# Optimization experiments

Hardware: AMD Instinct MI355X
Metric: run time of the kernel (lower is better)

## Reference

```python
import jax, jax.numpy as jnp
import numpy as np

N_NODES = 100000
EMBED_DIM = 256


def _sage_conv(x, src, dst, W_l, b_l, W_r, num_nodes):
    # PyG SAGEConv (mean aggr): out = lin_l(mean_{j in N(i)} x_j) + lin_r(x_i)
    msg = x[src]                                              # [E, D] gather
    agg = jax.ops.segment_sum(msg, dst, num_segments=num_nodes)   # [N, D]
    cnt = jax.ops.segment_sum(jnp.ones((src.shape[0], 1), x.dtype), dst,
                              num_segments=num_nodes)         # [N, 1]
    mean = agg / jnp.maximum(cnt, 1.0)
    return mean @ W_l + b_l + x @ W_r


def setup_inputs() -> dict:
    key = jax.random.key(0)
    ks = jax.random.split(key, 12)
    D = EMBED_DIM
    glorot = 1.0 / np.sqrt(D)
    inp = {
        "emb": jax.random.uniform(ks[0], (N_NODES + 1, D), jnp.float32, 0.001, 0.3),
        "W1l": jax.random.uniform(ks[1], (D, D), jnp.float32, -glorot, glorot),
        "b1l": jnp.zeros((D,), jnp.float32),
        "W1r": jax.random.uniform(ks[2], (D, D), jnp.float32, -glorot, glorot),
        "W2l": jax.random.uniform(ks[3], (D, D), jnp.float32, -glorot, glorot),
        "b2l": jnp.zeros((D,), jnp.float32),
        "W2r": jax.random.uniform(ks[4], (D, D), jnp.float32, -glorot, glorot),
        "x_idx": jax.random.randint(ks[5], (N_NODES,), 0, N_NODES + 1, jnp.int64 if jax.config.read('jax_enable_x64') else jnp.int32),
        "edge_index": jax.random.randint(ks[6], (2, 1600000), 0, N_NODES, jnp.int32),
        "drugNodes": jax.random.randint(ks[7], (1024,), 0, N_NODES, jnp.int32),
        "seNodes": jax.random.randint(ks[8], (1024,), 0, N_NODES, jnp.int32),
    }
    return inp


def reference(emb, W1l, b1l, W1r, W2l, b2l, W2r, x_idx, edge_index, drugNodes, seNodes):
    src, dst = edge_index[0], edge_index[1]
    x = emb[x_idx]                                            # embedding lookup [N, D]
    x = _sage_conv(x, src, dst, W1l, b1l, W1r, x.shape[0])
    x = _sage_conv(x, src, dst, W2l, b2l, W2r, x.shape[0])
    drugEmbedding = x[drugNodes]
    seEmbedding = x[seNodes]
    return (drugEmbedding, seEmbedding, x)
```

## Files before the change

kernel.cpp:

```cpp
#include <hip/hip_runtime.h>
#include <hip/hip_bf16.h>


typedef __bf16 bf16x8 __attribute__((ext_vector_type(8)));
typedef __bf16 bf16x4 __attribute__((ext_vector_type(4)));
typedef float  f32x4  __attribute__((ext_vector_type(4)));
typedef float  f32x8  __attribute__((ext_vector_type(8)));

#define ROWB 1024
#define NPART 256
#define MAXBUK 2048

__device__ __forceinline__ void async_copy16(void* lds_dst, const void* g_src) {
  __builtin_amdgcn_global_load_lds(
      (const __attribute__((address_space(1))) void*)g_src,
      (__attribute__((address_space(3))) void*)lds_dst, 16, 0, 0);
}


__global__ void bin_count(const int* __restrict__ dst, int* __restrict__ hmat,
                          int E, int chunk, int nbuk) {
  __shared__ int lh[MAXBUK];
  int p = blockIdx.x, tid = threadIdx.x;
  for (int i = tid; i < nbuk; i += 256) lh[i] = 0;
  __syncthreads();
  int base = p * chunk, end = min(base + chunk, E);
  for (int e = base + tid; e < end; e += 256) atomicAdd(&lh[dst[e] >> 6], 1);
  __syncthreads();
  for (int i = tid; i < nbuk; i += 256) hmat[p * nbuk + i] = lh[i];
}

__global__ void col_scan(int* __restrict__ hmat, int* __restrict__ btot, int nbuk) {
  __shared__ int s[NPART];
  int b = blockIdx.x, t = threadIdx.x;
  int v = hmat[t * nbuk + b];
  s[t] = v; __syncthreads();
  for (int d = 1; d < NPART; d <<= 1) {
    int add = (t >= d) ? s[t - d] : 0;
    __syncthreads();
    s[t] += add;
    __syncthreads();
  }
  hmat[t * nbuk + b] = s[t] - v;
  if (t == NPART - 1) btot[b] = s[t];
}

__global__ void bucket_scan(const int* __restrict__ btot, int* __restrict__ boff, int nb) {
  __shared__ int s[2048];
  int t = threadIdx.x;
  for (int i = t; i < 2048; i += 1024) s[i] = (i < nb) ? btot[i] : 0;
  __syncthreads();
  for (int d = 1; d < 2048; d <<= 1) {
    int v0 = (t >= d) ? s[t - d] : 0;
    int v1 = (t + 1024 >= d) ? s[t + 1024 - d] : 0;
    __syncthreads();
    s[t] += v0; s[t + 1024] += v1;
    __syncthreads();
  }
  for (int i = t; i < nb; i += 1024) boff[i] = s[i] - btot[i];
}

__global__ void part_write(const int* __restrict__ src, const int* __restrict__ dst,
                           const int* __restrict__ hmat, const int* __restrict__ boff,
                           int* __restrict__ ebuf, int E, int chunk, int nbuk) {
  __shared__ int cur[MAXBUK];
  int p = blockIdx.x, tid = threadIdx.x;
  for (int i = tid; i < nbuk; i += 256) cur[i] = hmat[p * nbuk + i] + boff[i];
  __syncthreads();
  int base = p * chunk, end = min(base + chunk, E);
  for (int e = base + tid; e < end; e += 256) {
    int d = dst[e];
    int pos = atomicAdd(&cur[d >> 6], 1);
    ebuf[pos] = src[e] | ((d & 63) << 18);
  }
}

__global__ void node_hist_scan(const int* __restrict__ ebuf, const int* __restrict__ boff,
                               const int* __restrict__ btot, int* __restrict__ cnt,
                               int* __restrict__ offs, int N) {
  __shared__ int lh[64];
  int b = blockIdx.x, tid = threadIdx.x;
  if (tid < 64) lh[tid] = 0;
  __syncthreads();
  int s0 = boff[b], s1 = s0 + btot[b];
  for (int i = s0 + tid; i < s1; i += 256) atomicAdd(&lh[ebuf[i] >> 18], 1);
  __syncthreads();
  if (tid < 64) {
    int v = lh[tid];
    int x = v;
#pragma unroll
    for (int d = 1; d < 64; d <<= 1) {
      int y = __shfl_up(x, d);
      if (tid >= d) x += y;
    }
    int node = b * 64 + tid;
    if (node < N) { cnt[node] = v; offs[node] = s0 + x - v; }
  }
}

__global__ void csr_write(const int* __restrict__ ebuf, const int* __restrict__ boff,
                          const int* __restrict__ btot, const int* __restrict__ offs,
                          int* __restrict__ csr, int N) {
  __shared__ int cur[64];
  int b = blockIdx.x, tid = threadIdx.x;
  int node = b * 64 + tid;
  if (tid < 64) cur[tid] = (node < N) ? offs[node] : 0;
  __syncthreads();
  int s0 = boff[b], s1 = s0 + btot[b];
  for (int i = s0 + tid; i < s1; i += 256) {
    int e = ebuf[i];
    int p = atomicAdd(&cur[e >> 18], 1);
    csr[p] = e & 0x3FFFF;
  }
}


__global__ void prep_w_kernel(const float* __restrict__ W1l, const float* __restrict__ W1r,
                              const float* __restrict__ W2l, const float* __restrict__ W2r,
                              __bf16* __restrict__ Wt1, __bf16* __restrict__ Wt2) {
  int idx = blockIdx.x * 256 + threadIdx.x;
  int which = idx >> 17;
  int j = idx & 131071;
  int n = j >> 9, k = j & 511;
  const float* Wl = which ? W2l : W1l;
  const float* Wr = which ? W2r : W1r;
  float v = (k < 256) ? Wl[k * 256 + n] : Wr[(k - 256) * 256 + n];
  (which ? Wt2 : Wt1)[j] = (__bf16)v;
}

__global__ void gather_x_kernel(const float* __restrict__ emb, const int* __restrict__ x_idx,
                                char* __restrict__ xbase, int N) {
  int wave = threadIdx.x >> 6, lane = threadIdx.x & 63;
  int i = blockIdx.x * 4 + wave;
  if (i >= N) return;
  int s = x_idx[i];
  float4 v = *(const float4*)(emb + (size_t)s * 256 + lane * 4);
  bf16x4 o = { (__bf16)v.x, (__bf16)v.y, (__bf16)v.z, (__bf16)v.w };
  *(bf16x4*)(xbase + (size_t)i * ROWB + lane * 8) = o;
}


__global__ void sage_agg(const char* __restrict__ srcbase,
                         char* __restrict__ dstbase,
                         const int* __restrict__ csr, const int* __restrict__ cnt,
                         const int* __restrict__ offs, int N) {
  int wave = threadIdx.x >> 6, lane = threadIdx.x & 63;
  int i = blockIdx.x * 4 + wave;
  if (i >= N) return;
  int deg = cnt[i];
  const int* lp = csr + offs[i];
  int half = lane >> 5, l5 = lane & 31;
  const char* sb = srcbase + l5 * 16;

  f32x8 acc = (f32x8)0.f;
  int g8 = deg >> 3;
  for (int t = 0; t < g8; ++t) {
    const int* p = lp + t * 8 + half;
    int s0 = p[0], s1 = p[2], s2 = p[4], s3 = p[6];
    bf16x8 v0 = *(const bf16x8*)(sb + (size_t)s0 * ROWB);
    bf16x8 v1 = *(const bf16x8*)(sb + (size_t)s1 * ROWB);
    bf16x8 v2 = *(const bf16x8*)(sb + (size_t)s2 * ROWB);
    bf16x8 v3 = *(const bf16x8*)(sb + (size_t)s3 * ROWB);
#pragma unroll
    for (int k = 0; k < 8; ++k)
      acc[k] += ((float)v0[k] + (float)v1[k]) + ((float)v2[k] + (float)v3[k]);
  }
  int base = g8 * 8;
  int rem = deg & 7;
  int rp = rem >> 1;
  for (int u = 0; u < rp; ++u) {
    int r0 = lp[base + 2 * u + half];
    bf16x8 v0 = *(const bf16x8*)(sb + (size_t)r0 * ROWB);
#pragma unroll
    for (int k = 0; k < 8; ++k) acc[k] += (float)v0[k];
  }
  if ((rem & 1) && half == 0) {
    int r0 = lp[deg - 1];
    bf16x8 v0 = *(const bf16x8*)(sb + (size_t)r0 * ROWB);
#pragma unroll
    for (int k = 0; k < 8; ++k) acc[k] += (float)v0[k];
  }

  float inv = 1.0f / (float)(deg > 0 ? deg : 1);
  bf16x8 o;
#pragma unroll
  for (int k = 0; k < 8; ++k) {
    float s = acc[k] + __shfl_down(acc[k], 32);
    o[k] = (__bf16)(s * inv);
  }
  if (half == 0)
    *(bf16x8*)(dstbase + (size_t)i * ROWB + l5 * 16) = o;
}


template <int OUT_F32>
__global__ __launch_bounds__(256) void gemm_sage(const char* __restrict__ Abase,
                                                 const __bf16* __restrict__ Wt,
                                                 const float* __restrict__ bias,
                                                 char* __restrict__ outbase, int M) {
  __shared__ __align__(16) char lds[49152];
  const int tid = threadIdx.x;
  const int wave = tid >> 6, lane = tid & 63;
  const int r = lane & 15, q = lane >> 4;
  const int wm = wave >> 1, wn = wave & 1;
  const int row0 = blockIdx.x * 128;

  f32x4 acc[4][8];
#pragma unroll
  for (int t = 0; t < 4; ++t)
#pragma unroll
    for (int u = 0; u < 8; ++u) acc[t][u] = (f32x4)0.f;

  auto stage = [&](int kk, int buf) {
    char* lbase = lds + buf * 24576;
#pragma unroll
    for (int i = 0; i < 2; ++i) {
      int h = wave * 2 + i;
      int rowA = row0 + h * 16 + r;
      rowA = rowA < M ? rowA : M - 1;
      async_copy16(lbase + h * 1024 + lane * 16,
                   Abase + (size_t)rowA * ROWB + (size_t)(kk * 32 + q * 8) * 2);
    }
#pragma unroll
    for (int i = 0; i < 4; ++i) {
      int h = wave * 4 + i;
      async_copy16(lbase + 8192 + h * 1024 + lane * 16,
                   (const char*)Wt + ((size_t)(h * 16 + r) * 512 + kk * 32 + q * 8) * 2);
    }
  };

  stage(0, 0);
  for (int kk = 0; kk < 16; ++kk) {
    __syncthreads();
    if (kk < 15) stage(kk + 1, (kk + 1) & 1);
    const char* lbase = lds + (kk & 1) * 24576;
    bf16x8 a[4];
#pragma unroll
    for (int t = 0; t < 4; ++t)
      a[t] = *(const bf16x8*)(lbase + (wm * 4 + t) * 1024 + lane * 16);
#pragma unroll
    for (int u = 0; u < 8; ++u) {
      bf16x8 b = *(const bf16x8*)(lbase + 8192 + (wn * 8 + u) * 1024 + lane * 16);
#pragma unroll
      for (int t = 0; t < 4; ++t)
        acc[t][u] = __builtin_amdgcn_mfma_f32_16x16x32_bf16(a[t], b, acc[t][u], 0, 0, 0);
    }
  }

#pragma unroll
  for (int t = 0; t < 4; ++t) {
    int rbase = row0 + wm * 64 + t * 16 + q * 4;
#pragma unroll
    for (int u = 0; u < 8; ++u) {
      int col = wn * 128 + u * 16 + r;
      float bv = bias[col];
#pragma unroll
      for (int j = 0; j < 4; ++j) {
        int row = rbase + j;
        if (row < M) {
          float v = acc[t][u][j] + bv;
          if (OUT_F32)
            *(float*)(outbase + (size_t)row * ROWB + col * 4) = v;
          else
            *(__bf16*)(outbase + (size_t)row * ROWB + 512 + col * 2) = (__bf16)v;
        }
      }
    }
  }
}


__global__ void gather_out_kernel(const float* __restrict__ x2, const int* __restrict__ drug,
                                  const int* __restrict__ se, float* __restrict__ out,
                                  int nd, int ns) {
  int wave = threadIdx.x >> 6, lane = threadIdx.x & 63;
  int ro = blockIdx.x * 4 + wave;
  if (ro >= nd + ns) return;
  int node = (ro < nd) ? drug[ro] : se[ro - nd];
  float4 v = *(const float4*)(x2 + (size_t)node * 256 + lane * 4);
  *(float4*)(out + (size_t)ro * 256 + lane * 4) = v;
}


extern "C" void kernel_launch(void* const* d_in, const int* in_sizes, int n_in,
                              void* d_out, int out_size, void* d_ws, size_t ws_size,
                              hipStream_t stream) {
  const float* emb  = (const float*)d_in[0];
  const float* W1l  = (const float*)d_in[1];
  const float* b1l  = (const float*)d_in[2];
  const float* W1r  = (const float*)d_in[3];
  const float* W2l  = (const float*)d_in[4];
  const float* b2l  = (const float*)d_in[5];
  const float* W2r  = (const float*)d_in[6];
  const int* x_idx  = (const int*)d_in[7];
  const int* edge   = (const int*)d_in[8];
  const int* drug   = (const int*)d_in[9];
  const int* se     = (const int*)d_in[10];

  const int N = in_sizes[7];
  const int E = in_sizes[8] / 2;
  const int nd = in_sizes[9], ns = in_sizes[10];
  const int* esrc = edge;
  const int* edst = edge + E;
  const int NBUK = (N + 63) >> 6;
  const int chunk = (E + NPART - 1) / NPART;

  char* ws = (char*)d_ws;
  size_t off = 0;
  char* xA1 = ws;                       off += (size_t)((N + 127) & ~127) * ROWB;
  __bf16* Wt1 = (__bf16*)(ws + off);    off += 512 * 256 * 2;
  __bf16* Wt2 = (__bf16*)(ws + off);    off += 512 * 256 * 2;
  int* cnt  = (int*)(ws + off);         off += ((size_t)N * 4 + 255) & ~(size_t)255;
  int* offs = (int*)(ws + off);         off += ((size_t)N * 4 + 255) & ~(size_t)255;
  int* csr  = (int*)(ws + off);         off += ((size_t)E * 4 + 255) & ~(size_t)255;
  int* ebuf = (int*)xA1;
  int* hmat = (int*)(xA1 + (8u << 20));
  int* btot = (int*)(xA1 + (16u << 20));
  int* boff = (int*)(xA1 + (16u << 20) + 16384);

  float* outp = (float*)d_out;
  float* x2 = outp + (size_t)(nd + ns) * 256;
  char* scratch2 = (char*)x2;

  const int QB = (N + 3) / 4;
  const int GB = (N + 127) / 128;

  prep_w_kernel<<<(2 * 131072) / 256, 256, 0, stream>>>(W1l, W1r, W2l, W2r, Wt1, Wt2);

  bin_count<<<NPART, 256, 0, stream>>>(edst, hmat, E, chunk, NBUK);
  col_scan<<<NBUK, NPART, 0, stream>>>(hmat, btot, NBUK);
  bucket_scan<<<1, 1024, 0, stream>>>(btot, boff, NBUK);
  part_write<<<NPART, 256, 0, stream>>>(esrc, edst, hmat, boff, ebuf, E, chunk, NBUK);
  node_hist_scan<<<NBUK, 256, 0, stream>>>(ebuf, boff, btot, cnt, offs, N);
  csr_write<<<NBUK, 256, 0, stream>>>(ebuf, boff, btot, offs, csr, N);

  gather_x_kernel<<<QB, 256, 0, stream>>>(emb, x_idx, xA1 + 512, N);
  sage_agg<<<QB, 256, 0, stream>>>(xA1 + 512, xA1, csr, cnt, offs, N);
  gemm_sage<0><<<GB, 256, 0, stream>>>(xA1, Wt1, b1l, scratch2, N);
  sage_agg<<<QB, 256, 0, stream>>>(scratch2 + 512, scratch2, csr, cnt, offs, N);
  gemm_sage<1><<<GB, 256, 0, stream>>>(scratch2, Wt2, b2l, scratch2, N);

  gather_out_kernel<<<(nd + ns + 3) / 4, 256, 0, stream>>>(x2, drug, se, outp, nd, ns);
}
```

Baseline: 639.0 us.

## Load GEMM operands directly into registers and fuse node histogram with CSR write

```diff
diff --git a/kernel.cpp b/kernel.cpp
--- a/kernel.cpp
+++ b/kernel.cpp
@@ -10,12 +10,6 @@
 #define ROWB 1024
 #define NPART 256
 #define MAXBUK 2048
-
-__device__ __forceinline__ void async_copy16(void* lds_dst, const void* g_src) {
-  __builtin_amdgcn_global_load_lds(
-      (const __attribute__((address_space(1))) void*)g_src,
-      (__attribute__((address_space(3))) void*)lds_dst, 16, 0, 0);
-}
 
 
 __global__ void bin_count(const int* __restrict__ dst, int* __restrict__ hmat,
@@ -75,10 +69,11 @@
   }
 }
 
-__global__ void node_hist_scan(const int* __restrict__ ebuf, const int* __restrict__ boff,
-                               const int* __restrict__ btot, int* __restrict__ cnt,
-                               int* __restrict__ offs, int N) {
+__global__ void hist_csr(const int* __restrict__ ebuf, const int* __restrict__ boff,
+                         const int* __restrict__ btot, int* __restrict__ cnt,
+                         int* __restrict__ offs, int* __restrict__ csr, int N) {
   __shared__ int lh[64];
+  __shared__ int cur[64];
   int b = blockIdx.x, tid = threadIdx.x;
   if (tid < 64) lh[tid] = 0;
   __syncthreads();
@@ -93,20 +88,12 @@
       int y = __shfl_up(x, d);
       if (tid >= d) x += y;
     }
+    int o = s0 + x - v;
+    cur[tid] = o;
     int node = b * 64 + tid;
-    if (node < N) { cnt[node] = v; offs[node] = s0 + x - v; }
-  }
-}
-
-__global__ void csr_write(const int* __restrict__ ebuf, const int* __restrict__ boff,
-                          const int* __restrict__ btot, const int* __restrict__ offs,
-                          int* __restrict__ csr, int N) {
-  __shared__ int cur[64];
-  int b = blockIdx.x, tid = threadIdx.x;
-  int node = b * 64 + tid;
-  if (tid < 64) cur[tid] = (node < N) ? offs[node] : 0;
-  __syncthreads();
-  int s0 = boff[b], s1 = s0 + btot[b];
+    if (node < N) { cnt[node] = v; offs[node] = o; }
+  }
+  __syncthreads();
   for (int i = s0 + tid; i < s1; i += 256) {
     int e = ebuf[i];
     int p = atomicAdd(&cur[e >> 18], 1);
@@ -121,7 +108,10 @@
   int idx = blockIdx.x * 256 + threadIdx.x;
   int which = idx >> 17;
   int j = idx & 131071;
-  int n = j >> 9, k = j & 511;
+  int kkq = j >> 11;
+  int n = (j >> 3) & 255;
+  int e = j & 7;
+  int k = (kkq >> 2) * 32 + (kkq & 3) * 8 + e;
   const float* Wl = which ? W2l : W1l;
   const float* Wr = which ? W2r : W1r;
   float v = (k < 256) ? Wl[k * 256 + n] : Wr[(k - 256) * 256 + n];
@@ -195,10 +185,9 @@
 
 template <int OUT_F32>
 __global__ __launch_bounds__(256) void gemm_sage(const char* __restrict__ Abase,
-                                                 const __bf16* __restrict__ Wt,
+                                                 const __bf16* __restrict__ WtB,
                                                  const float* __restrict__ bias,
                                                  char* __restrict__ outbase, int M) {
-  __shared__ __align__(16) char lds[49152];
   const int tid = threadIdx.x;
   const int wave = tid >> 6, lane = tid & 63;
   const int r = lane & 15, q = lane >> 4;
@@ -211,40 +200,28 @@
 #pragma unroll
     for (int u = 0; u < 8; ++u) acc[t][u] = (f32x4)0.f;
 
-  auto stage = [&](int kk, int buf) {
-    char* lbase = lds + buf * 24576;
-#pragma unroll
-    for (int i = 0; i < 2; ++i) {
-      int h = wave * 2 + i;
-      int rowA = row0 + h * 16 + r;
-      rowA = rowA < M ? rowA : M - 1;
-      async_copy16(lbase + h * 1024 + lane * 16,
-                   Abase + (size_t)rowA * ROWB + (size_t)(kk * 32 + q * 8) * 2);
-    }
-#pragma unroll
-    for (int i = 0; i < 4; ++i) {
-      int h = wave * 4 + i;
-      async_copy16(lbase + 8192 + h * 1024 + lane * 16,
-                   (const char*)Wt + ((size_t)(h * 16 + r) * 512 + kk * 32 + q * 8) * 2);
-    }
-  };
-
-  stage(0, 0);
+  const char* aptr[4];
+#pragma unroll
+  for (int t = 0; t < 4; ++t) {
+    int rowA = row0 + (wm * 4 + t) * 16 + r;
+    rowA = rowA < M ? rowA : M - 1;
+    aptr[t] = Abase + (size_t)rowA * ROWB + q * 16;
+  }
+  const char* bbase = (const char*)WtB + ((size_t)q * 256 + wn * 128 + r) * 16;
+
   for (int kk = 0; kk < 16; ++kk) {
-    __syncthreads();
-    if (kk < 15) stage(kk + 1, (kk + 1) & 1);
-    const char* lbase = lds + (kk & 1) * 24576;
-    bf16x8 a[4];
+    bf16x8 a[4], b[8];
 #pragma unroll
     for (int t = 0; t < 4; ++t)
-      a[t] = *(const bf16x8*)(lbase + (wm * 4 + t) * 1024 + lane * 16);
-#pragma unroll
-    for (int u = 0; u < 8; ++u) {
-      bf16x8 b = *(const bf16x8*)(lbase + 8192 + (wn * 8 + u) * 1024 + lane * 16);
+      a[t] = *(const bf16x8*)(aptr[t] + kk * 64);
+#pragma unroll
+    for (int u = 0; u < 8; ++u)
+      b[u] = *(const bf16x8*)(bbase + kk * 16384 + u * 256);
+#pragma unroll
+    for (int u = 0; u < 8; ++u)
 #pragma unroll
       for (int t = 0; t < 4; ++t)
-        acc[t][u] = __builtin_amdgcn_mfma_f32_16x16x32_bf16(a[t], b, acc[t][u], 0, 0, 0);
-    }
+        acc[t][u] = __builtin_amdgcn_mfma_f32_16x16x32_bf16(a[t], b[u], acc[t][u], 0, 0, 0);
   }
 
 #pragma unroll
@@ -331,8 +308,7 @@
   col_scan<<<NBUK, NPART, 0, stream>>>(hmat, btot, NBUK);
   bucket_scan<<<1, 1024, 0, stream>>>(btot, boff, NBUK);
   part_write<<<NPART, 256, 0, stream>>>(esrc, edst, hmat, boff, ebuf, E, chunk, NBUK);
-  node_hist_scan<<<NBUK, 256, 0, stream>>>(ebuf, boff, btot, cnt, offs, N);
-  csr_write<<<NBUK, 256, 0, stream>>>(ebuf, boff, btot, offs, csr, N);
+  hist_csr<<<NBUK, 256, 0, stream>>>(ebuf, boff, btot, cnt, offs, csr, N);
 
   gather_x_kernel<<<QB, 256, 0, stream>>>(emb, x_idx, xA1 + 512, N);
   sage_agg<<<QB, 256, 0, stream>>>(xA1 + 512, xA1, csr, cnt, offs, N);
```

Measured after the change: 762.5 us. +19.3%, slower.
